# Kernel tuning notes

Measured on AMD Instinct MI355X. Metric: run time of the kernel, lower is better.

The kernel has to match this reference:

```python
import jax, jax.numpy as jnp
import numpy as np

P = 16  # num_partitions
DIN = 256  # in_features // P
DOUT = 256  # out_features // P

def setup_inputs() -> dict:
    key = jax.random.key(0)
    k1, k2, k3 = jax.random.split(key, 3)
    inputs = jax.random.normal(k1, (8, 2048, P * DIN), dtype=jnp.float32)
    weight = jax.random.normal(k2, (P, DOUT, DIN), dtype=jnp.float32) * (1.0 / np.sqrt(DIN))
    bias = jax.random.normal(k3, (P * DOUT,), dtype=jnp.float32) * (1.0 / np.sqrt(DIN))
    return {"inputs": inputs, "weight": weight, "bias": bias}

def reference(inputs, weight, bias):
    # inputs: (B, S, P*DIN) -> (B, S, P, DIN)
    x = inputs.reshape(*inputs.shape[:-1], P, DIN)
    # block-diagonal matmul: (B,S,P,DIN) x (P,DOUT,DIN) -> (B,S,P,DOUT)
    y = jnp.einsum('bspi,poi->bspo', x, weight)
    # transpose=True: swap (P, DOUT) -> (DOUT, P), then flatten
    y = jnp.swapaxes(y, -2, -1)
    y = y.reshape(*y.shape[:-2], DOUT * P)
    return y + bias
```

## Files before the change

kernel.cpp:

```cpp
#include <hip/hip_runtime.h>


typedef __attribute__((ext_vector_type(4))) float f32x4;
typedef __attribute__((ext_vector_type(8))) short short8;

#define LDS_ROW 8208
#define LDS_SIZE (16 * LDS_ROW)

__device__ __forceinline__ unsigned int pk2(float a, float b) {
  union { float f; unsigned int u; } x, y;
  x.f = a; y.f = b;
  unsigned int ua = x.u + (0x7fffu + ((x.u >> 16) & 1u));
  unsigned int ub = y.u + (0x7fffu + ((y.u >> 16) & 1u));
  return (ua >> 16) | (ub & 0xffff0000u);
}

__global__ __launch_bounds__(256) void wconv_kernel(
    const float* __restrict__ w, unsigned int* __restrict__ o) {
  int i = blockIdx.x * 256 + threadIdx.x;
  float4 f = ((const float4*)w)[i];
  uint2 u;
  u.x = pk2(f.x, f.y);
  u.y = pk2(f.z, f.w);
  ((uint2*)o)[i] = u;
}

__global__ __launch_bounds__(1024, 1) void diag_gemm_kernel(
    const float* __restrict__ x, const unsigned short* __restrict__ wb,
    const float* __restrict__ bias, float* __restrict__ out) {
  extern __shared__ char lds[];
  const int tid = threadIdx.x;
  const int wv  = tid >> 6;
  const int l   = tid & 63;
  const long T0 = (long)blockIdx.x * 16;

  {
    const float* src = x + (T0 + wv) * 4096;
    char* dst = lds + wv * LDS_ROW;
#pragma unroll
    for (int i = 0; i < 8; ++i) {
      int c = l + 64 * i;
      float4 f0 = ((const float4*)src)[2 * c];
      float4 f1 = ((const float4*)src)[2 * c + 1];
      uint4 u;
      u.x = pk2(f0.x, f0.y);
      u.y = pk2(f0.z, f0.w);
      u.z = pk2(f1.x, f1.y);
      u.w = pk2(f1.z, f1.w);
      *(uint4*)(dst + c * 16) = u;
    }
  }
  __syncthreads();

  const int n  = l & 15;
  const int kg = l >> 4;
  const int o0 = wv * 16;

  const char* abase = lds + n * LDS_ROW + kg * 16;
  const unsigned short* bbase = wb + (o0 + n) * 256 + kg * 8;
  float* obase = out + T0 * 4096 + (long)(o0 + n) * 16;
  const float* bptr = bias + (o0 + n) * 16;

#pragma unroll
  for (int pg = 0; pg < 4; ++pg) {
    f32x4 acc[4];
#pragma unroll
    for (int pi = 0; pi < 4; ++pi) acc[pi] = (f32x4){0.f, 0.f, 0.f, 0.f};

#pragma unroll
    for (int pi = 0; pi < 4; ++pi) {
      const int p = pg * 4 + pi;
      const char* ap = abase + p * 512;
      const unsigned short* bp = bbase + p * 65536;
      short8 a[8], b[8];
#pragma unroll
      for (int ks = 0; ks < 8; ++ks) {
        a[ks] = *(const short8*)(ap + ks * 64);
        b[ks] = *(const short8*)(bp + ks * 32);
      }
#pragma unroll
      for (int ks = 0; ks < 8; ++ks)
        acc[pi] = __builtin_amdgcn_mfma_f32_16x16x32_bf16(a[ks], b[ks], acc[pi], 0, 0, 0);
    }

    float4 bv = *(const float4*)(bptr + pg * 4);
#pragma unroll
    for (int r = 0; r < 4; ++r) {
      int m = kg * 4 + r;
      float4 v = make_float4(acc[0][r] + bv.x, acc[1][r] + bv.y,
                             acc[2][r] + bv.z, acc[3][r] + bv.w);
      *(float4*)(obase + (long)m * 4096 + pg * 4) = v;
    }
  }
}

extern "C" void kernel_launch(void* const* d_in, const int* in_sizes, int n_in,
                              void* d_out, int out_size, void* d_ws, size_t ws_size,
                              hipStream_t stream) {
  const float* x    = (const float*)d_in[0];
  const float* w    = (const float*)d_in[1];
  const float* bias = (const float*)d_in[2];
  float* out = (float*)d_out;
  unsigned int* wb = (unsigned int*)d_ws;

  (void)hipFuncSetAttribute((const void*)diag_gemm_kernel,
                            hipFuncAttributeMaxDynamicSharedMemorySize, LDS_SIZE);

  wconv_kernel<<<1024, 256, 0, stream>>>(w, wb);

  diag_gemm_kernel<<<1024, 1024, LDS_SIZE, stream>>>(
      x, (const unsigned short*)wb, bias, out);
}
```

Baseline: 722.0 us.

## Halve block size, double-buffer A/B fragments and prefetch weights before staging

Moves from 1024-thread blocks to 512-thread blocks with two blocks per CU, so each wave handles two output column groups and two staged input rows. It adds a register double-buffer that prefetches the next partition's A (LDS) and B (global) fragments while the current MFMA chain runs, and issues the first weight load before the LDS staging barrier. Each output row is now written as four contiguous float4 stores. The aim is to hide load latency and overlap blocks at the barrier, at the cost of a larger register footprint (two fragment buffers plus 16 accumulators) that could cause spills at the 512x2 launch bound.

Measured after the change: 673.5 us. 6.7% less time.

```diff
diff --git a/kernel.cpp b/kernel.cpp
--- a/kernel.cpp
+++ b/kernel.cpp
@@ -25,7 +25,7 @@
   ((uint2*)o)[i] = u;
 }
 
-__global__ __launch_bounds__(1024, 1) void diag_gemm_kernel(
+__global__ __launch_bounds__(512, 2) void diag_gemm_kernel(
     const float* __restrict__ x, const unsigned short* __restrict__ wb,
     const float* __restrict__ bias, float* __restrict__ out) {
   extern __shared__ char lds[];
@@ -34,9 +34,22 @@
   const int l   = tid & 63;
   const long T0 = (long)blockIdx.x * 16;
 
-  {
-    const float* src = x + (T0 + wv) * 4096;
-    char* dst = lds + wv * LDS_ROW;
+  const int n  = l & 15;
+  const int kg = l >> 4;
+
+  const unsigned short* bbs0 = wb + (wv * 16 + n) * 256 + kg * 8;
+  const unsigned short* bbs1 = wb + ((wv + 8) * 16 + n) * 256 + kg * 8;
+
+  short8 a[2][8], b[2][8];
+
+#pragma unroll
+  for (int ks = 0; ks < 8; ++ks) b[0][ks] = *(const short8*)(bbs0 + ks * 32);
+
+#pragma unroll
+  for (int rr = 0; rr < 2; ++rr) {
+    const int row = wv * 2 + rr;
+    const float* src = x + (T0 + row) * 4096;
+    char* dst = lds + row * LDS_ROW;
 #pragma unroll
     for (int i = 0; i < 8; ++i) {
       int c = l + 64 * i;
@@ -52,44 +65,62 @@
   }
   __syncthreads();
 
-  const int n  = l & 15;
-  const int kg = l >> 4;
-  const int o0 = wv * 16;
+  const char* abase = lds + n * LDS_ROW + kg * 16;
+#pragma unroll
+  for (int ks = 0; ks < 8; ++ks) a[0][ks] = *(const short8*)(abase + ks * 64);
 
-  const char* abase = lds + n * LDS_ROW + kg * 16;
-  const unsigned short* bbase = wb + (o0 + n) * 256 + kg * 8;
-  float* obase = out + T0 * 4096 + (long)(o0 + n) * 16;
-  const float* bptr = bias + (o0 + n) * 16;
+  float* obase = out + T0 * 4096;
 
 #pragma unroll
-  for (int pg = 0; pg < 4; ++pg) {
-    f32x4 acc[4];
-#pragma unroll
-    for (int pi = 0; pi < 4; ++pi) acc[pi] = (f32x4){0.f, 0.f, 0.f, 0.f};
+  for (int s = 0; s < 2; ++s) {
+    const int o0 = (wv + 8 * s) * 16;
+    f32x4 res[16];
 
 #pragma unroll
-    for (int pi = 0; pi < 4; ++pi) {
-      const int p = pg * 4 + pi;
-      const char* ap = abase + p * 512;
-      const unsigned short* bp = bbase + p * 65536;
-      short8 a[8], b[8];
+    for (int p = 0; p < 16; ++p) {
+      const int g = s * 16 + p;
+      const int cur = g & 1, nxt = cur ^ 1;
+      if (g < 31) {
+        const int gn = g + 1;
+        const unsigned short* bp =
+            ((gn & 16) ? bbs1 : bbs0) + (gn & 15) * 65536;
 #pragma unroll
-      for (int ks = 0; ks < 8; ++ks) {
-        a[ks] = *(const short8*)(ap + ks * 64);
-        b[ks] = *(const short8*)(bp + ks * 32);
+        for (int ks = 0; ks < 8; ++ks)
+          b[nxt][ks] = *(const short8*)(bp + ks * 32);
+        const char* ap = abase + (gn & 15) * 512;
+#pragma unroll
+        for (int ks = 0; ks < 8; ++ks)
+          a[nxt][ks] = *(const short8*)(ap + ks * 64);
       }
+      f32x4 acc = (f32x4){0.f, 0.f, 0.f, 0.f};
 #pragma unroll
       for (int ks = 0; ks < 8; ++ks)
-        acc[pi] = __builtin_amdgcn_mfma_f32_16x16x32_bf16(a[ks], b[ks], acc[pi], 0, 0, 0);
+        acc = __builtin_amdgcn_mfma_f32_16x16x32_bf16(a[cur][ks], b[cur][ks],
+                                                      acc, 0, 0, 0);
+      res[p] = acc;
     }
 
-    float4 bv = *(const float4*)(bptr + pg * 4);
+    const float* bp2 = bias + (o0 + n) * 16;
+    float4 bv0 = ((const float4*)bp2)[0];
+    float4 bv1 = ((const float4*)bp2)[1];
+    float4 bv2 = ((const float4*)bp2)[2];
+    float4 bv3 = ((const float4*)bp2)[3];
+    float* ob = obase + (long)(o0 + n) * 16;
 #pragma unroll
     for (int r = 0; r < 4; ++r) {
-      int m = kg * 4 + r;
-      float4 v = make_float4(acc[0][r] + bv.x, acc[1][r] + bv.y,
-                             acc[2][r] + bv.z, acc[3][r] + bv.w);
-      *(float4*)(obase + (long)m * 4096 + pg * 4) = v;
+      float* orow = ob + (long)(kg * 4 + r) * 4096;
+      float4 v0 = make_float4(res[0][r] + bv0.x, res[1][r] + bv0.y,
+                              res[2][r] + bv0.z, res[3][r] + bv0.w);
+      float4 v1 = make_float4(res[4][r] + bv1.x, res[5][r] + bv1.y,
+                              res[6][r] + bv1.z, res[7][r] + bv1.w);
+      float4 v2 = make_float4(res[8][r] + bv2.x, res[9][r] + bv2.y,
+                              res[10][r] + bv2.z, res[11][r] + bv2.w);
+      float4 v3 = make_float4(res[12][r] + bv3.x, res[13][r] + bv3.y,
+                              res[14][r] + bv3.z, res[15][r] + bv3.w);
+      ((float4*)orow)[0] = v0;
+      ((float4*)orow)[1] = v1;
+      ((float4*)orow)[2] = v2;
+      ((float4*)orow)[3] = v3;
     }
   }
 }
@@ -108,6 +139,6 @@
 
   wconv_kernel<<<1024, 256, 0, stream>>>(w, wb);
 
-  diag_gemm_kernel<<<1024, 1024, LDS_SIZE, stream>>>(
+  diag_gemm_kernel<<<1024, 512, LDS_SIZE, stream>>>(
       x, (const unsigned short*)wb, bias, out);
 }
```
